# Kernel optimization log

Hardware: AMD Instinct MI355X
Metric: run time of the kernel (lower is better)

Reference implementation:

```python
import jax, jax.numpy as jnp
import numpy as np

H = 8; C = 128; P_E = 128; P_D = 64
N = 10000; E = 100000; B = 32
NEG_SLOPE = 0.01  # torch.nn.LeakyReLU default


def setup_inputs() -> dict:
    key = jax.random.key(0)
    ks = jax.random.split(key, 20)
    def lin(k, din, dout):
        return jax.random.normal(k, (din, dout), jnp.float32) / np.float32(np.sqrt(din))
    inp = dict(
        x=jax.random.normal(ks[0], (N, P_E), jnp.float32),
        index=jax.random.randint(ks[1], (2, E), 0, N),
        attr=jax.random.normal(ks[2], (E, P_D), jnp.float32),
        batch=jnp.sort(jax.random.randint(ks[3], (N,), 0, B)),
    )
    i = 4
    for l in (1, 2):
        inp[f"Wq{l}"] = lin(ks[i], P_E, H * C); i += 1
        inp[f"bq{l}"] = jnp.zeros((H * C,), jnp.float32)
        inp[f"Wk{l}"] = lin(ks[i], P_E, H * C); i += 1
        inp[f"bk{l}"] = jnp.zeros((H * C,), jnp.float32)
        inp[f"Wv{l}"] = lin(ks[i], P_E, H * C); i += 1
        inp[f"bv{l}"] = jnp.zeros((H * C,), jnp.float32)
        inp[f"We{l}"] = lin(ks[i], P_D, H * C); i += 1  # lin_edge, bias=False in PyG
        inp[f"Wskip{l}"] = lin(ks[i], P_E, P_E); i += 1  # root/skip linear (concat=False)
        inp[f"bskip{l}"] = jnp.zeros((P_E,), jnp.float32)
        inp[f"gnw{l}"] = jnp.ones((P_E,), jnp.float32)   # GraphNorm weight
        inp[f"gnb{l}"] = jnp.zeros((P_E,), jnp.float32)  # GraphNorm bias
        inp[f"gnm{l}"] = jnp.ones((P_E,), jnp.float32)   # GraphNorm mean_scale
    return inp


def transformer_conv(x, src, dst, attr, Wq, bq, Wk, bk, Wv, bv, We, Wskip, bskip):
    # PyG TransformerConv: heads=H, out_channels=C, concat=False, edge_dim=P_D,
    # dropout inactive (eval). Messages flow src=edge_index[0] -> dst=edge_index[1].
    q = (x @ Wq + bq).reshape(N, H, C)
    k = (x @ Wk + bk).reshape(N, H, C)
    v = (x @ Wv + bv).reshape(N, H, C)
    e = (attr @ We).reshape(E, H, C)
    kj = k[src] + e                                                   # [E,H,C]
    alpha = jnp.einsum('ehc,ehc->eh', q[dst], kj) / np.float32(np.sqrt(C))
    # segment softmax over destination node (numerically stable)
    amax = jax.ops.segment_max(alpha, dst, num_segments=N)            # [N,H]
    ex = jnp.exp(alpha - amax[dst])
    denom = jax.ops.segment_sum(ex, dst, num_segments=N)
    w = ex / (denom[dst] + 1e-16)                                     # [E,H]
    msg = (v[src] + e) * w[:, :, None]                                # [E,H,C]
    out = jax.ops.segment_sum(msg, dst, num_segments=N)               # [N,H,C]
    out = out.mean(axis=1)                                            # concat=False -> head mean
    return out + x @ Wskip + bskip                                    # root_weight=True


def graph_norm(x, batch, w, b, ms, eps=1e-5):
    cnt = jnp.maximum(jax.ops.segment_sum(jnp.ones((N,), x.dtype), batch, num_segments=B), 1.0)
    mean = jax.ops.segment_sum(x, batch, num_segments=B) / cnt[:, None]
    out = x - mean[batch] * ms
    var = jax.ops.segment_sum(out * out, batch, num_segments=B) / cnt[:, None]
    return out / jnp.sqrt(var[batch] + eps) * w + b


def reference(x, index, attr, batch,
              Wq1, bq1, Wk1, bk1, Wv1, bv1, We1, Wskip1, bskip1, gnw1, gnb1, gnm1,
              Wq2, bq2, Wk2, bk2, Wv2, bv2, We2, Wskip2, bskip2, gnw2, gnb2, gnm2):
    src, dst = index[0], index[1]
    h = transformer_conv(x, src, dst, attr, Wq1, bq1, Wk1, bk1, Wv1, bv1, We1, Wskip1, bskip1)
    h = jax.nn.leaky_relu(graph_norm(h, batch, gnw1, gnb1, gnm1), NEG_SLOPE)
    h = transformer_conv(h, src, dst, attr, Wq2, bq2, Wk2, bk2, Wv2, bv2, We2, Wskip2, bskip2)
    return jax.nn.leaky_relu(graph_norm(h, batch, gnw2, gnb2, gnm2), NEG_SLOPE)
```

## Files before the change

kernel.cpp:

```cpp
#include <hip/hip_runtime.h>
#include <hip/hip_bf16.h>
#include <math.h>

#define NN 10000
#define NE 100000
#define NB 32

typedef __attribute__((ext_vector_type(8))) short short8;
typedef __attribute__((ext_vector_type(4))) float f32x4;
typedef __attribute__((ext_vector_type(2))) float f32x2;
typedef _Float16 h2 __attribute__((ext_vector_type(2)));

union H8 { short8 s; h2 h[4]; };
union HU { _Float16 h; ushort u; };

__device__ inline ushort f2b(float f) {
  union { float f; unsigned u; } a; a.f = f;
  unsigned r = a.u + 0x7fff + ((a.u >> 16) & 1);
  return (ushort)(r >> 16);
}
__device__ inline float bf2f(ushort u) {
  union { unsigned u; float f; } a; a.u = ((unsigned)u) << 16;
  return a.f;
}
__device__ inline ushort f2h(float f) { HU x; x.h = (_Float16)f; return x.u; }
__device__ inline float h2f(ushort u) { HU x; x.u = u; return (float)x.h; }

__device__ inline float e4m3_sw(unsigned b) {
  unsigned s = b & 0x80, e = (b >> 3) & 15, m = b & 7;
  float v = (e == 0) ? (float)m * (1.f / 512.f) : ldexpf((float)(8 + m), (int)e - 10);
  return s ? -v : v;
}
__device__ inline unsigned f2e4m3_sw(float f) {
  unsigned s = (__float_as_uint(f) >> 24) & 0x80;
  float a = fabsf(f);
  if (a < 0.0009765625f) return s;
  if (a >= 448.f) return s | 0x7e;
  if (a < 0.015625f) {
    int q = (int)rintf(a * 512.f);
    return s | (unsigned)q;
  }
  int e2; frexpf(a, &e2);
  int sh = e2 - 4;
  int M = (int)rintf(ldexpf(a, -sh));
  if (M >= 16) { M >>= 1; sh++; }
  int E = sh + 10;
  if (E > 15) return s | 0x7e;
  return s | (unsigned)((E << 3) | (M - 8));
}

#if defined(__has_builtin)
#if __has_builtin(__builtin_amdgcn_cvt_pk_f32_fp8) && __has_builtin(__builtin_amdgcn_cvt_pk_fp8_f32)
#define HW_FP8 1
#endif
#endif

#ifdef HW_FP8
template <bool HI>
__device__ inline f32x2 dec2(unsigned w) {
  return __builtin_amdgcn_cvt_pk_f32_fp8((int)w, HI);
}
template <bool HI>
__device__ inline unsigned enc2(float a, float b, unsigned old) {
  return (unsigned)__builtin_amdgcn_cvt_pk_fp8_f32(a, b, (int)old, HI);
}
#else
template <bool HI>
__device__ inline f32x2 dec2(unsigned w) {
  unsigned x = HI ? (w >> 16) : (w & 0xffff);
  f32x2 r; r[0] = e4m3_sw(x & 0xff); r[1] = e4m3_sw((x >> 8) & 0xff);
  return r;
}
template <bool HI>
__device__ inline unsigned enc2(float a, float b, unsigned old) {
  unsigned pk = f2e4m3_sw(a) | (f2e4m3_sw(b) << 8);
  return HI ? ((old & 0xffffu) | (pk << 16)) : ((old & 0xffff0000u) | pk);
}
#endif

#if defined(__has_builtin)
#if __has_builtin(__builtin_amdgcn_fdot2)
#define FDOT2(a, b, c) __builtin_amdgcn_fdot2((a), (b), (c), false)
#endif
#endif
#ifndef FDOT2
#define FDOT2(a, b, c) ((c) + (float)(a)[0] * (float)(b)[0] + (float)(a)[1] * (float)(b)[1])
#endif

#define GLDS(g, l)                                                        \
  __builtin_amdgcn_global_load_lds(                                       \
      (const __attribute__((address_space(1))) unsigned*)(g),             \
      (__attribute__((address_space(3))) unsigned*)(l), 16, 0, 0)

__global__ __launch_bounds__(256) void k_gemm_qkvt(
    const ushort* __restrict__ Abf, const ushort* __restrict__ Bt,
    const float* __restrict__ bias, ushort* __restrict__ qt,
    unsigned char* __restrict__ kv8, int M) {
  __shared__ ushort As[128 * 128];
  __shared__ ushort Bs[128 * 128];
  const int tid = threadIdx.x;
  const int l = tid & 63, w = tid >> 6;
  const int wm = w & 1, wn = w >> 1;
  const int row0 = blockIdx.y * 128, col0 = blockIdx.x * 128;
#pragma unroll
  for (int i = 0; i < 8; ++i) {
    int idx = i * 256 + tid;
    int r = idx >> 4, cb = (idx & 15) << 4;
    int scb = cb ^ ((r & 7) << 4);
    GLDS((const char*)Abf + (size_t)(row0 + r) * 256 + scb, (char*)As + idx * 16);
    GLDS((const char*)Bt + (size_t)(col0 + r) * 256 + scb, (char*)Bs + idx * 16);
  }
  __syncthreads();
  f32x4 acc[4][4] = {};
#pragma unroll
  for (int kk = 0; kk < 4; ++kk) {
    short8 af[4], bf[4];
#pragma unroll
    for (int fm = 0; fm < 4; ++fm) {
      int r = wm * 64 + fm * 16 + (l & 15);
      int cb = (kk * 64 + ((l >> 4) << 4)) ^ ((r & 7) << 4);
      af[fm] = *(const short8*)((const char*)As + r * 256 + cb);
    }
#pragma unroll
    for (int fn = 0; fn < 4; ++fn) {
      int r = wn * 64 + fn * 16 + (l & 15);
      int cb = (kk * 64 + ((l >> 4) << 4)) ^ ((r & 7) << 4);
      bf[fn] = *(const short8*)((const char*)Bs + r * 256 + cb);
    }
#pragma unroll
    for (int fm = 0; fm < 4; ++fm)
#pragma unroll
      for (int fn = 0; fn < 4; ++fn)
        acc[fm][fn] = __builtin_amdgcn_mfma_f32_16x16x32_bf16(af[fm], bf[fn], acc[fm][fn], 0, 0, 0);
  }
  __syncthreads();
#pragma unroll
  for (int fm = 0; fm < 4; ++fm) {
    int rloc = wm * 64 + fm * 16 + ((l >> 4) << 2);
#pragma unroll
    for (int fn = 0; fn < 4; ++fn) {
      int cbyte = (wn * 64 + fn * 16 + (l & 15)) * 2;
#pragma unroll
      for (int b = 0; b < 4; ++b) {
        int r = rloc + b;
        *(ushort*)((char*)As + r * 256 + (cbyte ^ ((r & 7) << 4))) = f2h(acc[fm][fn][b]);
      }
    }
  }
  __syncthreads();
  const bool isf16 = (col0 < 1024) || (col0 >= 3072);
#pragma unroll
  for (int it = 0; it < 8; ++it) {
    int idx = it * 256 + tid;
    int r = idx >> 4, cb16 = (idx & 15) << 4;
    int gr = row0 + r;
    if (gr >= M) continue;
    short8 v = *(const short8*)((const char*)As + r * 256 + (cb16 ^ ((r & 7) << 4)));
    int co = cb16 >> 1;
    if (isf16) {
      int qc0 = ((col0 < 1024) ? col0 : (col0 - 2048)) + co;
      short8 o;
#pragma unroll
      for (int j = 0; j < 8; ++j) o[j] = (short)f2h(h2f((ushort)v[j]) + bias[col0 + co + j]);
      *(short8*)(qt + (size_t)gr * 1536 + qc0) = o;
    } else {
      float f[8];
#pragma unroll
      for (int j = 0; j < 8; ++j) f[j] = h2f((ushort)v[j]) + bias[col0 + co + j];
      unsigned w0 = 0, w1 = 0;
      w0 = enc2<false>(f[0], f[1], w0);
      w0 = enc2<true>(f[2], f[3], w0);
      w1 = enc2<false>(f[4], f[5], w1);
      w1 = enc2<true>(f[6], f[7], w1);
      uint2 st; st.x = w0; st.y = w1;
      *(uint2*)(kv8 + (size_t)gr * 2048 + (col0 - 1024) + co) = st;
    }
  }
}

__global__ __launch_bounds__(256) void k_gemm_out(
    const ushort* __restrict__ s_b, const ushort* __restrict__ xin,
    const ushort* __restrict__ W2t, const ushort* __restrict__ Wsk,
    const float* __restrict__ bsk, const float* __restrict__ mbuf,
    float* __restrict__ Cf, int M) {
  __shared__ ushort As[128 * 128];
  __shared__ ushort Bs[128 * 128];
  const int tid = threadIdx.x;
  const int l = tid & 63, w = tid >> 6;
  const int wm = w & 1, wn = w >> 1;
  const int row0 = blockIdx.y * 128;
  f32x4 acc[4][4] = {};
  for (int kt = 0; kt < 5; ++kt) {
    if (kt) __syncthreads();
    const char* Ab; const char* Bb; size_t arb, brb; int ko;
    if (kt < 4) { Ab = (const char*)s_b; arb = 1024; Bb = (const char*)W2t; brb = 1024; ko = kt * 256; }
    else        { Ab = (const char*)xin; arb = 256;  Bb = (const char*)Wsk; brb = 256;  ko = 0; }
#pragma unroll
    for (int i = 0; i < 8; ++i) {
      int idx = i * 256 + tid;
      int r = idx >> 4, cb = (idx & 15) << 4;
      int scb = cb ^ ((r & 7) << 4);
      GLDS(Ab + (size_t)(row0 + r) * arb + ko + scb, (char*)As + idx * 16);
      GLDS(Bb + (size_t)r * brb + ko + scb, (char*)Bs + idx * 16);
    }
    __syncthreads();
#pragma unroll
    for (int kk = 0; kk < 4; ++kk) {
      short8 af[4], bf[4];
#pragma unroll
      for (int fm = 0; fm < 4; ++fm) {
        int r = wm * 64 + fm * 16 + (l & 15);
        int cb = (kk * 64 + ((l >> 4) << 4)) ^ ((r & 7) << 4);
        af[fm] = *(const short8*)((const char*)As + r * 256 + cb);
      }
#pragma unroll
      for (int fn = 0; fn < 4; ++fn) {
        int r = wn * 64 + fn * 16 + (l & 15);
        int cb = (kk * 64 + ((l >> 4) << 4)) ^ ((r & 7) << 4);
        bf[fn] = *(const short8*)((const char*)Bs + r * 256 + cb);
      }
#pragma unroll
      for (int fm = 0; fm < 4; ++fm)
#pragma unroll
        for (int fn = 0; fn < 4; ++fn)
          acc[fm][fn] = __builtin_amdgcn_mfma_f32_16x16x32_bf16(af[fm], bf[fn], acc[fm][fn], 0, 0, 0);
    }
  }
#pragma unroll
  for (int fm = 0; fm < 4; ++fm) {
    int row = row0 + wm * 64 + fm * 16 + ((l >> 4) << 2);
#pragma unroll
    for (int fn = 0; fn < 4; ++fn) {
      int col = wn * 64 + fn * 16 + (l & 15);
      if (col >= 128) continue;
      float bb = bsk[col];
#pragma unroll
      for (int b = 0; b < 4; ++b) {
        int rr = row + b;
        if (rr >= M) continue;
        Cf[(size_t)rr * 128 + col] = acc[fm][fn][b] + bb + mbuf[(size_t)rr * 128 + col];
      }
    }
  }
}

struct WtPrep { const float* W[8]; ushort* O[8]; int Nc[8]; };
__global__ void k_wt_all(WtPrep P) {
  const int z = blockIdx.z;
  const int Nc = P.Nc[z];
  if ((int)blockIdx.x * 32 >= Nc) return;
  const float* __restrict__ W = P.W[z];
  ushort* __restrict__ Wt = P.O[z];
  __shared__ float tile[32][33];
  const int t = threadIdx.x, lx = t & 31, ly = t >> 5;
  const int bx = blockIdx.x, by = blockIdx.y;
#pragma unroll
  for (int i = 0; i < 4; ++i)
    tile[ly + i * 8][lx] = W[(by * 32 + ly + i * 8) * Nc + bx * 32 + lx];
  __syncthreads();
#pragma unroll
  for (int i = 0; i < 4; ++i)
    Wt[(size_t)(bx * 32 + ly + i * 8) * 128 + by * 32 + lx] = f2b(tile[lx][ly + i * 8]);
}

struct PrepPtrs {
  const float* Wq[2]; const float* We[2]; ushort* Mt[2];
  const float* bq[2]; const float* bk[2]; const float* bv[2];
  ushort* W2t[2]; float* biasAll[2];
};

__global__ __launch_bounds__(256) void k_mwt(PrepPtrs P) {
  const int L = blockIdx.y;
  const float* __restrict__ Wq = P.Wq[L];
  const float* __restrict__ We = P.We[L];
  ushort* __restrict__ Mt = P.Mt[L];
  const int h = blockIdx.x >> 3, pt = blockIdx.x & 7;
  const int t = threadIdx.x;
  __shared__ float Wes[64][129];
  __shared__ float Wqs[16][129];
#pragma unroll
  for (int i = 0; i < 32; ++i) {
    int idx = i * 256 + t;
    Wes[idx >> 7][idx & 127] = We[(idx >> 7) * 1024 + h * 128 + (idx & 127)];
  }
#pragma unroll
  for (int i = 0; i < 8; ++i) {
    int idx = i * 256 + t;
    Wqs[idx >> 7][idx & 127] = Wq[(pt * 16 + (idx >> 7)) * 1024 + h * 128 + (idx & 127)];
  }
  __syncthreads();
#pragma unroll
  for (int i = 0; i < 4; ++i) {
    int o = i * 256 + t;
    int d = o & 63, p = o >> 6;
    float s = 0.f;
#pragma unroll 8
    for (int c = 0; c < 128; ++c) s += Wqs[p][c] * Wes[d][c];
    Mt[(size_t)(h * 64 + d) * 128 + pt * 16 + p] = f2b(s);
  }
}

__global__ void k_w2t(PrepPtrs P) {
  const int L = blockIdx.y;
  int o = blockIdx.x * 256 + threadIdx.x;
  if (o < 128 * 512) {
    int c = o >> 9, hd = o & 511;
    int hh = hd >> 6, d = hd & 63;
    P.W2t[L][o] = f2b(P.We[L][d * 1024 + hh * 128 + c] * 0.125f);
  }
}

__global__ void k_bias_all(PrepPtrs P) {
  const int L = blockIdx.y;
  int o = blockIdx.x * 256 + threadIdx.x;
  if (o < 1024) P.biasAll[L][o] = P.bq[L][o];
  else if (o < 2048) P.biasAll[L][o] = P.bk[L][o - 1024];
  else if (o < 3072) P.biasAll[L][o] = P.bv[L][o - 2048];
  else if (o < 3584) {
    int hd = o - 3072;
    int h = hd >> 6, d = hd & 63;
    float s = 0.f;
    for (int c = 0; c < 128; ++c) s += P.bq[L][h * 128 + c] * P.We[L][d * 1024 + h * 128 + c];
    P.biasAll[L][o] = s;
  }
}

__global__ void k_cvt(const float* __restrict__ in, ushort* __restrict__ out, int n4) {
  int i = blockIdx.x * 256 + threadIdx.x;
  if (i < n4) {
    float4 v = *(const float4*)(in + i * 4);
    ushort4 o;
    o.x = f2b(v.x); o.y = f2b(v.y); o.z = f2b(v.z); o.w = f2b(v.w);
    *(ushort4*)(out + i * 4) = o;
  }
}

__global__ void k_histo(const int* __restrict__ dst, int* __restrict__ cnt) {
  int e = blockIdx.x * 256 + threadIdx.x;
  if (e < NE) atomicAdd(&cnt[dst[e]], 1);
}

__global__ __launch_bounds__(256) void k_scan(const int* __restrict__ cnt,
                                              int* __restrict__ ptr) {
  __shared__ int tsum[256];
  const int t = threadIdx.x;
  const int base = t * 40;
  int s = 0;
  for (int i = 0; i < 40; ++i) { int idx = base + i; if (idx < NN) s += cnt[idx]; }
  tsum[t] = s;
  __syncthreads();
  for (int off = 1; off < 256; off <<= 1) {
    int v = (t >= off) ? tsum[t - off] : 0;
    __syncthreads();
    tsum[t] += v;
    __syncthreads();
  }
  int run = (t == 0) ? 0 : tsum[t - 1];
  for (int i = 0; i < 40; ++i) {
    int idx = base + i;
    if (idx < NN) { ptr[idx] = run; run += cnt[idx]; }
  }
  if (t == 255) ptr[NN] = tsum[255];
}

__global__ void k_scatter(const int* __restrict__ dst, const int* __restrict__ ptr,
                          int* __restrict__ cnt, int* __restrict__ eid) {
  int e = blockIdx.x * 256 + threadIdx.x;
  if (e < NE) {
    int d = dst[e];
    int pos = ptr[d] + atomicSub(&cnt[d], 1) - 1;
    eid[pos] = e;
  }
}

__global__ __launch_bounds__(256) void k_sortdeg(const int* __restrict__ ptr,
                                                 int* __restrict__ order) {
  __shared__ int hist[256];
  __shared__ int offs[256];
  __shared__ int fill[256];
  __shared__ int sc[256];
  const int t = threadIdx.x;
  hist[t] = 0;
  __syncthreads();
  for (int n = t; n < NN; n += 256) {
    int d = min(ptr[n + 1] - ptr[n], 255);
    atomicAdd(&hist[d], 1);
  }
  __syncthreads();
  const int rd = 255 - t;
  int v = hist[rd];
  sc[t] = v;
  __syncthreads();
  for (int off = 1; off < 256; off <<= 1) {
    int u = (t >= off) ? sc[t - off] : 0;
    __syncthreads();
    sc[t] += u;
    __syncthreads();
  }
  offs[rd] = sc[t] - v;
  fill[rd] = 0;
  __syncthreads();
  for (int n = t; n < NN; n += 256) {
    int d = min(ptr[n + 1] - ptr[n], 255);
    int pos = offs[d] + atomicAdd(&fill[d], 1);
    order[pos] = n;
  }
}

__global__ void k_permattr(const int* __restrict__ eid, const int* __restrict__ src,
                           const float* __restrict__ attr, int* __restrict__ src_p,
                           ushort* __restrict__ attr_p) {
  int i = blockIdx.x * 256 + threadIdx.x;
  if (i >= NE * 16) return;
  int idx = i >> 4, part = i & 15;
  int e = eid[idx];
  if (part == 0) src_p[idx] = src[e];
  float4 v = *(const float4*)(attr + (size_t)e * 64 + part * 4);
  ushort4 o;
  o.x = f2h(v.x); o.y = f2h(v.y); o.z = f2h(v.z); o.w = f2h(v.w);
  *(ushort4*)(attr_p + (size_t)idx * 64 + part * 4) = o;
}

__global__ void k_bptr(const int* __restrict__ batch, int* __restrict__ bptr) {
  int b = threadIdx.x;
  if (b > NB) return;
  int lo = 0, hi = NN;
  while (lo < hi) { int mid = (lo + hi) >> 1; if (batch[mid] < b) lo = mid + 1; else hi = mid; }
  bptr[b] = lo;
}

__global__ __launch_bounds__(256) void k_fused(
    const ushort* __restrict__ qt, const unsigned char* __restrict__ kv8,
    const ushort* __restrict__ attr_p, const int* __restrict__ src_p,
    const int* __restrict__ ptr, const int* __restrict__ order,
    float* __restrict__ mbuf, ushort* __restrict__ s_b) {
  const int slot = blockIdx.x * 4 + (threadIdx.x >> 6);
  if (slot >= NN) return;
  const int n = order[slot];
  const int l = threadIdx.x & 63;
  const int i = l & 7;
  float qf[16];
  {
    H8 q0, q1;
    const ushort* qr = qt + (size_t)n * 1536 + l * 16;
    q0.s = *(const short8*)qr;
    q1.s = *(const short8*)(qr + 8);
#pragma unroll
    for (int j = 0; j < 8; ++j) { qf[j] = h2f((ushort)q0.s[j]); qf[8 + j] = h2f((ushort)q1.s[j]); }
  }
  H8 tv;
  tv.s = *(const short8*)(qt + (size_t)n * 1536 + 1024 + l * 8);
  const int beg = ptr[n], end = ptr[n + 1];
  float m = -1e30f, den = 0.f;
  float acc[16] = {};
  float sa[8] = {};
  uint4 kw, vw; H8 av;
  if (beg < end) {
    int s0 = src_p[beg];
    const unsigned char* kr = kv8 + (size_t)s0 * 2048 + l * 16;
    kw = *(const uint4*)kr;
    vw = *(const uint4*)(kr + 1024);
    av.s = *(const short8*)(attr_p + (size_t)beg * 64 + i * 8);
  }
  for (int idx = beg; idx < end; ++idx) {
    uint4 ckw = kw, cvw = vw; H8 cav = av;
    int nidx = (idx + 1 < end) ? idx + 1 : idx;
    int ns = src_p[nidx];
    const unsigned char* kr = kv8 + (size_t)ns * 2048 + l * 16;
    kw = *(const uint4*)kr;
    vw = *(const uint4*)(kr + 1024);
    av.s = *(const short8*)(attr_p + (size_t)nidx * 64 + i * 8);
    float p = 0.f;
    {
      const unsigned* kws = (const unsigned*)&ckw;
#pragma unroll
      for (int j = 0; j < 4; ++j) {
        f32x2 lo = dec2<false>(kws[j]), hi = dec2<true>(kws[j]);
        p += qf[4 * j] * lo[0] + qf[4 * j + 1] * lo[1]
           + qf[4 * j + 2] * hi[0] + qf[4 * j + 3] * hi[1];
      }
    }
#pragma unroll
    for (int j = 0; j < 4; ++j) p = FDOT2(tv.h[j], cav.h[j], p);
    p += __shfl_xor(p, 1, 64);
    p += __shfl_xor(p, 2, 64);
    p += __shfl_xor(p, 4, 64);
    p *= 0.12751593061420927f;
    float mn = fmaxf(m, p);
    float r = exp2f(m - mn);
    float ex = exp2f(p - mn);
    den = den * r + ex;
    {
      const unsigned* vws = (const unsigned*)&cvw;
#pragma unroll
      for (int j = 0; j < 4; ++j) {
        f32x2 lo = dec2<false>(vws[j]), hi = dec2<true>(vws[j]);
        acc[4 * j]     = acc[4 * j]     * r + ex * lo[0];
        acc[4 * j + 1] = acc[4 * j + 1] * r + ex * lo[1];
        acc[4 * j + 2] = acc[4 * j + 2] * r + ex * hi[0];
        acc[4 * j + 3] = acc[4 * j + 3] * r + ex * hi[1];
      }
    }
#pragma unroll
    for (int j = 0; j < 4; ++j) {
      sa[2 * j]     = sa[2 * j]     * r + ex * (float)cav.h[j][0];
      sa[2 * j + 1] = sa[2 * j + 1] * r + ex * (float)cav.h[j][1];
    }
    m = mn;
  }
  const float invd = den > 0.f ? 1.f / den : 0.f;
  short8 sb;
#pragma unroll
  for (int j = 0; j < 8; ++j) sb[j] = (short)f2b(sa[j] * invd);
  *(short8*)(s_b + (size_t)n * 512 + l * 8) = sb;
#pragma unroll
  for (int j = 0; j < 16; ++j) {
    float a = acc[j] * invd;
    a += __shfl_xor(a, 8, 64);
    a += __shfl_xor(a, 16, 64);
    a += __shfl_xor(a, 32, 64);
    acc[j] = a;
  }
  if (l < 8) {
    float* mb = mbuf + (size_t)n * 128 + l * 16;
#pragma unroll
    for (int j = 0; j < 16; j += 4) {
      float4 o = make_float4(acc[j] * 0.125f, acc[j + 1] * 0.125f,
                             acc[j + 2] * 0.125f, acc[j + 3] * 0.125f);
      *(float4*)(mb + j) = o;
    }
  }
}

__global__ __launch_bounds__(256) void k_gn_partial(
    const float* __restrict__ x, const int* __restrict__ bptr,
    float* __restrict__ gs, float* __restrict__ gs2) {
  const int b = blockIdx.x >> 2, chunk = blockIdx.x & 3;
  const int t = threadIdx.x;
  const int c = t & 127, half = t >> 7;
  const int beg = bptr[b], end = bptr[b + 1];
  float s = 0.f, s2 = 0.f;
  for (int n = beg + chunk * 2 + half; n < end; n += 8) {
    float v = x[(size_t)n * 128 + c];
    s += v; s2 += v * v;
  }
  __shared__ float r1[256];
  __shared__ float r2[256];
  r1[t] = s; r2[t] = s2;
  __syncthreads();
  if (half == 0) {
    atomicAdd(&gs[b * 128 + c], r1[c] + r1[c + 128]);
    atomicAdd(&gs2[b * 128 + c], r2[c] + r2[c + 128]);
  }
}

__global__ void k_gn_apply(const float* __restrict__ x, const int* __restrict__ batch,
                           const int* __restrict__ bptr,
                           const float* __restrict__ gs, const float* __restrict__ gs2,
                           const float* __restrict__ ms, const float* __restrict__ wgt,
                           const float* __restrict__ gnb,
                           float* __restrict__ fout, ushort* __restrict__ bout) {
  int i = blockIdx.x * 256 + threadIdx.x;
  int n = i >> 7, c = i & 127;
  int b = batch[n];
  float cnt = fmaxf((float)(bptr[b + 1] - bptr[b]), 1.f);
  float mean = gs[b * 128 + c] / cnt;
  float mm = mean * ms[c];
  float var = gs2[b * 128 + c] / cnt - 2.f * mm * mean + mm * mm;
  float o = (x[i] - mm) * rsqrtf(var + 1e-5f) * wgt[c] + gnb[c];
  o = o > 0.f ? o : 0.01f * o;
  if (fout) fout[i] = o;
  if (bout) bout[i] = f2b(o);
}

extern "C" void kernel_launch(void* const* d_in, const int* in_sizes, int n_in,
                              void* d_out, int out_size, void* d_ws, size_t ws_size,
                              hipStream_t stream) {
  const float* x     = (const float*)d_in[0];
  const int*   index = (const int*)d_in[1];
  const float* attr  = (const float*)d_in[2];
  const int*   batch = (const int*)d_in[3];
  const int* srcArr = index;
  const int* dstArr = index + NE;

  char* p = (char*)d_ws;
  auto take = [&](size_t bytes) {
    char* r = p;
    p += (bytes + 255) & ~(size_t)255;
    return (void*)r;
  };
  ushort* qt_b   = (ushort*)take((size_t)NN * 1536 * 2);
  unsigned char* kv8 = (unsigned char*)take((size_t)NN * 2048);
  ushort* s_b    = (ushort*)take((size_t)NN * 512 * 2);
  float*  mbuf   = (float*)take((size_t)NN * 128 * 4);
  float*  hbuf   = (float*)take((size_t)NN * 128 * 4);
  ushort* xb     = (ushort*)take((size_t)NN * 128 * 2);
  ushort* x2b    = (ushort*)take((size_t)NN * 128 * 2);
  ushort* attr_p = (ushort*)take((size_t)NE * 64 * 2);
  int*    src_p  = (int*)take((size_t)NE * 4);
  float*  gsum   = (float*)take((size_t)NB * 128 * 2 * 4);
  int* csr_ptr   = (int*)take((size_t)(NN + 1) * 4);
  int* csr_cnt   = (int*)take((size_t)NN * 4);
  int* csr_eid   = (int*)take((size_t)NE * 4);
  int* nodeorder = (int*)take((size_t)NN * 4);
  int* bptrd     = (int*)take((size_t)(NB + 1) * 4);
  float* gs  = gsum;
  float* gs2 = gsum + NB * 128;
  ushort* WtAll[2]; ushort* Wtsk[2]; ushort* W2t[2];
  float* biasAll[2];
  for (int L = 0; L < 2; ++L) {
    WtAll[L]   = (ushort*)take((size_t)3584 * 128 * 2);
    Wtsk[L]    = (ushort*)take((size_t)128 * 128 * 2);
    W2t[L]     = (ushort*)take((size_t)128 * 512 * 2);
    biasAll[L] = (float*)take((size_t)3584 * 4);
  }

  hipMemsetAsync(csr_cnt, 0, NN * 4, stream);
  k_histo<<<(NE + 255) / 256, 256, 0, stream>>>(dstArr, csr_cnt);
  k_scan<<<1, 256, 0, stream>>>(csr_cnt, csr_ptr);
  k_scatter<<<(NE + 255) / 256, 256, 0, stream>>>(dstArr, csr_ptr, csr_cnt, csr_eid);
  k_sortdeg<<<1, 256, 0, stream>>>(csr_ptr, nodeorder);
  k_permattr<<<(NE * 16 + 255) / 256, 256, 0, stream>>>(csr_eid, srcArr, attr, src_p, attr_p);
  k_bptr<<<1, 64, 0, stream>>>(batch, bptrd);
  k_cvt<<<(NN * 128 / 4 + 255) / 256, 256, 0, stream>>>(x, xb, NN * 128 / 4);

  WtPrep WP;
  PrepPtrs PP;
  for (int L = 0; L < 2; ++L) {
    const float* Wq  = (const float*)d_in[4 + L * 12 + 0];
    const float* bq  = (const float*)d_in[4 + L * 12 + 1];
    const float* Wk  = (const float*)d_in[4 + L * 12 + 2];
    const float* bk  = (const float*)d_in[4 + L * 12 + 3];
    const float* Wv  = (const float*)d_in[4 + L * 12 + 4];
    const float* bv  = (const float*)d_in[4 + L * 12 + 5];
    const float* We  = (const float*)d_in[4 + L * 12 + 6];
    const float* Wsk = (const float*)d_in[4 + L * 12 + 7];
    WP.W[L * 4 + 0] = Wq;  WP.O[L * 4 + 0] = WtAll[L];                      WP.Nc[L * 4 + 0] = 1024;
    WP.W[L * 4 + 1] = Wk;  WP.O[L * 4 + 1] = WtAll[L] + (size_t)1024 * 128; WP.Nc[L * 4 + 1] = 1024;
    WP.W[L * 4 + 2] = Wv;  WP.O[L * 4 + 2] = WtAll[L] + (size_t)2048 * 128; WP.Nc[L * 4 + 2] = 1024;
    WP.W[L * 4 + 3] = Wsk; WP.O[L * 4 + 3] = Wtsk[L];                       WP.Nc[L * 4 + 3] = 128;
    PP.Wq[L] = Wq; PP.We[L] = We; PP.Mt[L] = WtAll[L] + (size_t)3072 * 128;
    PP.bq[L] = bq; PP.bk[L] = bk; PP.bv[L] = bv;
    PP.W2t[L] = W2t[L]; PP.biasAll[L] = biasAll[L];
  }
  k_wt_all<<<dim3(32, 4, 8), 256, 0, stream>>>(WP);
  k_mwt<<<dim3(64, 2), 256, 0, stream>>>(PP);
  k_w2t<<<dim3(256, 2), 256, 0, stream>>>(PP);
  k_bias_all<<<dim3(14, 2), 256, 0, stream>>>(PP);

  const int MT = (NN + 127) / 128;
  for (int L = 0; L < 2; ++L) {
    const float* bsk = (const float*)d_in[4 + L * 12 + 8];
    const float* gnw = (const float*)d_in[4 + L * 12 + 9];
    const float* gnb = (const float*)d_in[4 + L * 12 + 10];
    const float* gnm = (const float*)d_in[4 + L * 12 + 11];
    const ushort* Ain = (L == 0) ? xb : x2b;

    k_gemm_qkvt<<<dim3(28, MT), 256, 0, stream>>>(Ain, WtAll[L], biasAll[L], qt_b, kv8, NN);
    k_fused<<<(NN + 3) / 4, 256, 0, stream>>>(qt_b, kv8, attr_p, src_p, csr_ptr, nodeorder, mbuf, s_b);
    k_gemm_out<<<dim3(1, MT), 256, 0, stream>>>(s_b, Ain, W2t[L], Wtsk[L], bsk, mbuf, hbuf, NN);
    hipMemsetAsync(gsum, 0, (size_t)NB * 128 * 2 * 4, stream);
    k_gn_partial<<<NB * 4, 256, 0, stream>>>(hbuf, bptrd, gs, gs2);
    k_gn_apply<<<NN * 128 / 256, 256, 0, stream>>>(
        hbuf, batch, bptrd, gs, gs2, gnm, gnw, gnb,
        (L == 0) ? (float*)nullptr : (float*)d_out,
        (L == 0) ? x2b : (ushort*)nullptr);
  }
}
```

Baseline: 314.7 us.

## Read GEMM B fragments from global, deepen edge prefetch, drop GraphNorm atomics

Both GEMM kernels stop staging the weight (B) tile in shared memory and read B fragments straight from global memory, which halves LDS use and may allow more resident blocks, but it issues many uncoalesced per-lane global loads inside the MFMA loop. The fused attention kernel now prefetches two edges ahead instead of one, with the source index loaded three ahead, to hide gather latency. GraphNorm partial sums are written to per-chunk slots that the apply kernel adds up, replacing the atomics and the memset launch.

```diff
diff --git a/kernel.cpp b/kernel.cpp
--- a/kernel.cpp
+++ b/kernel.cpp
@@ -97,7 +97,6 @@
     const float* __restrict__ bias, ushort* __restrict__ qt,
     unsigned char* __restrict__ kv8, int M) {
   __shared__ ushort As[128 * 128];
-  __shared__ ushort Bs[128 * 128];
   const int tid = threadIdx.x;
   const int l = tid & 63, w = tid >> 6;
   const int wm = w & 1, wn = w >> 1;
@@ -108,7 +107,6 @@
     int r = idx >> 4, cb = (idx & 15) << 4;
     int scb = cb ^ ((r & 7) << 4);
     GLDS((const char*)Abf + (size_t)(row0 + r) * 256 + scb, (char*)As + idx * 16);
-    GLDS((const char*)Bt + (size_t)(col0 + r) * 256 + scb, (char*)Bs + idx * 16);
   }
   __syncthreads();
   f32x4 acc[4][4] = {};
@@ -124,8 +122,7 @@
 #pragma unroll
     for (int fn = 0; fn < 4; ++fn) {
       int r = wn * 64 + fn * 16 + (l & 15);
-      int cb = (kk * 64 + ((l >> 4) << 4)) ^ ((r & 7) << 4);
-      bf[fn] = *(const short8*)((const char*)Bs + r * 256 + cb);
+      bf[fn] = *(const short8*)((const char*)Bt + (size_t)(col0 + r) * 256 + kk * 64 + ((l >> 4) << 4));
     }
 #pragma unroll
     for (int fm = 0; fm < 4; ++fm)
@@ -184,7 +181,6 @@
     const float* __restrict__ bsk, const float* __restrict__ mbuf,
     float* __restrict__ Cf, int M) {
   __shared__ ushort As[128 * 128];
-  __shared__ ushort Bs[128 * 128];
   const int tid = threadIdx.x;
   const int l = tid & 63, w = tid >> 6;
   const int wm = w & 1, wn = w >> 1;
@@ -201,7 +197,6 @@
       int r = idx >> 4, cb = (idx & 15) << 4;
       int scb = cb ^ ((r & 7) << 4);
       GLDS(Ab + (size_t)(row0 + r) * arb + ko + scb, (char*)As + idx * 16);
-      GLDS(Bb + (size_t)r * brb + ko + scb, (char*)Bs + idx * 16);
     }
     __syncthreads();
 #pragma unroll
@@ -216,8 +211,7 @@
 #pragma unroll
       for (int fn = 0; fn < 4; ++fn) {
         int r = wn * 64 + fn * 16 + (l & 15);
-        int cb = (kk * 64 + ((l >> 4) << 4)) ^ ((r & 7) << 4);
-        bf[fn] = *(const short8*)((const char*)Bs + r * 256 + cb);
+        bf[fn] = *(const short8*)(Bb + (size_t)r * brb + ko + kk * 64 + ((l >> 4) << 4));
       }
 #pragma unroll
       for (int fm = 0; fm < 4; ++fm)
@@ -454,22 +448,33 @@
   float m = -1e30f, den = 0.f;
   float acc[16] = {};
   float sa[8] = {};
-  uint4 kw, vw; H8 av;
+  uint4 k0, v0, k1, v1; H8 a0, a1;
+  int sC = 0;
   if (beg < end) {
-    int s0 = src_p[beg];
-    const unsigned char* kr = kv8 + (size_t)s0 * 2048 + l * 16;
-    kw = *(const uint4*)kr;
-    vw = *(const uint4*)(kr + 1024);
-    av.s = *(const short8*)(attr_p + (size_t)beg * 64 + i * 8);
-  }
+    const int last = end - 1;
+    int sA = src_p[beg];
+    const unsigned char* kr = kv8 + (size_t)sA * 2048 + l * 16;
+    k0 = *(const uint4*)kr;
+    v0 = *(const uint4*)(kr + 1024);
+    a0.s = *(const short8*)(attr_p + (size_t)beg * 64 + i * 8);
+    int i1 = min(beg + 1, last);
+    int sB = src_p[i1];
+    kr = kv8 + (size_t)sB * 2048 + l * 16;
+    k1 = *(const uint4*)kr;
+    v1 = *(const uint4*)(kr + 1024);
+    a1.s = *(const short8*)(attr_p + (size_t)i1 * 64 + i * 8);
+    sC = src_p[min(beg + 2, last)];
+  }
+  const int last = end - 1;
   for (int idx = beg; idx < end; ++idx) {
-    uint4 ckw = kw, cvw = vw; H8 cav = av;
-    int nidx = (idx + 1 < end) ? idx + 1 : idx;
-    int ns = src_p[nidx];
-    const unsigned char* kr = kv8 + (size_t)ns * 2048 + l * 16;
-    kw = *(const uint4*)kr;
-    vw = *(const uint4*)(kr + 1024);
-    av.s = *(const short8*)(attr_p + (size_t)nidx * 64 + i * 8);
+    uint4 ckw = k0, cvw = v0; H8 cav = a0;
+    k0 = k1; v0 = v1; a0 = a1;
+    int i2 = min(idx + 2, last);
+    const unsigned char* kr = kv8 + (size_t)sC * 2048 + l * 16;
+    k1 = *(const uint4*)kr;
+    v1 = *(const uint4*)(kr + 1024);
+    a1.s = *(const short8*)(attr_p + (size_t)i2 * 64 + i * 8);
+    sC = src_p[min(idx + 3, last)];
     float p = 0.f;
     {
       const unsigned* kws = (const unsigned*)&ckw;
@@ -534,7 +539,7 @@
 
 __global__ __launch_bounds__(256) void k_gn_partial(
     const float* __restrict__ x, const int* __restrict__ bptr,
-    float* __restrict__ gs, float* __restrict__ gs2) {
+    float* __restrict__ part) {
   const int b = blockIdx.x >> 2, chunk = blockIdx.x & 3;
   const int t = threadIdx.x;
   const int c = t & 127, half = t >> 7;
@@ -549,24 +554,29 @@
   r1[t] = s; r2[t] = s2;
   __syncthreads();
   if (half == 0) {
-    atomicAdd(&gs[b * 128 + c], r1[c] + r1[c + 128]);
-    atomicAdd(&gs2[b * 128 + c], r2[c] + r2[c + 128]);
+    part[((size_t)chunk * NB + b) * 128 + c] = r1[c] + r1[c + 128];
+    part[4 * NB * 128 + ((size_t)chunk * NB + b) * 128 + c] = r2[c] + r2[c + 128];
   }
 }
 
 __global__ void k_gn_apply(const float* __restrict__ x, const int* __restrict__ batch,
-                           const int* __restrict__ bptr,
-                           const float* __restrict__ gs, const float* __restrict__ gs2,
+                           const int* __restrict__ bptr, const float* __restrict__ part,
                            const float* __restrict__ ms, const float* __restrict__ wgt,
                            const float* __restrict__ gnb,
                            float* __restrict__ fout, ushort* __restrict__ bout) {
   int i = blockIdx.x * 256 + threadIdx.x;
   int n = i >> 7, c = i & 127;
   int b = batch[n];
+  float S = 0.f, S2 = 0.f;
+#pragma unroll
+  for (int ch = 0; ch < 4; ++ch) {
+    S  += part[((size_t)ch * NB + b) * 128 + c];
+    S2 += part[4 * NB * 128 + ((size_t)ch * NB + b) * 128 + c];
+  }
   float cnt = fmaxf((float)(bptr[b + 1] - bptr[b]), 1.f);
-  float mean = gs[b * 128 + c] / cnt;
+  float mean = S / cnt;
   float mm = mean * ms[c];
-  float var = gs2[b * 128 + c] / cnt - 2.f * mm * mean + mm * mm;
+  float var = S2 / cnt - 2.f * mm * mean + mm * mm;
   float o = (x[i] - mm) * rsqrtf(var + 1e-5f) * wgt[c] + gnb[c];
   o = o > 0.f ? o : 0.01f * o;
   if (fout) fout[i] = o;
@@ -598,14 +608,12 @@
   ushort* x2b    = (ushort*)take((size_t)NN * 128 * 2);
   ushort* attr_p = (ushort*)take((size_t)NE * 64 * 2);
   int*    src_p  = (int*)take((size_t)NE * 4);
-  float*  gsum   = (float*)take((size_t)NB * 128 * 2 * 4);
+  float*  part   = (float*)take((size_t)4 * NB * 128 * 2 * 4);
   int* csr_ptr   = (int*)take((size_t)(NN + 1) * 4);
   int* csr_cnt   = (int*)take((size_t)NN * 4);
   int* csr_eid   = (int*)take((size_t)NE * 4);
   int* nodeorder = (int*)take((size_t)NN * 4);
   int* bptrd     = (int*)take((size_t)(NB + 1) * 4);
-  float* gs  = gsum;
-  float* gs2 = gsum + NB * 128;
   ushort* WtAll[2]; ushort* Wtsk[2]; ushort* W2t[2];
   float* biasAll[2];
   for (int L = 0; L < 2; ++L) {
@@ -659,10 +667,9 @@
     k_gemm_qkvt<<<dim3(28, MT), 256, 0, stream>>>(Ain, WtAll[L], biasAll[L], qt_b, kv8, NN);
     k_fused<<<(NN + 3) / 4, 256, 0, stream>>>(qt_b, kv8, attr_p, src_p, csr_ptr, nodeorder, mbuf, s_b);
     k_gemm_out<<<dim3(1, MT), 256, 0, stream>>>(s_b, Ain, W2t[L], Wtsk[L], bsk, mbuf, hbuf, NN);
-    hipMemsetAsync(gsum, 0, (size_t)NB * 128 * 2 * 4, stream);
-    k_gn_partial<<<NB * 4, 256, 0, stream>>>(hbuf, bptrd, gs, gs2);
+    k_gn_partial<<<NB * 4, 256, 0, stream>>>(hbuf, bptrd, part);
     k_gn_apply<<<NN * 128 / 256, 256, 0, stream>>>(
-        hbuf, batch, bptrd, gs, gs2, gnm, gnw, gnb,
+        hbuf, batch, bptrd, part, gnm, gnw, gnb,
         (L == 0) ? (float*)nullptr : (float*)d_out,
         (L == 0) ? x2b : (ushort*)nullptr);
   }
```

Measured after the change: 338.3 us. +7.5%, slower.
